# Kernel tuning notes

Hardware: AMD Instinct MI355X
Metric: run time of the kernel (lower is better)

Reference implementation:

```python
import jax, jax.numpy as jnp
import numpy as np

B, T, N, D = 8, 512, 64, 128
PRED, HEADS, HID = 96, 8, 256
KERNELS = (17, 49)
NUM_LAYERS = 1
NUM_BLOCKS = 1
IDX_T = np.arange(64)   # lowest 64 of T//2=256 rfft modes (mode_select='low')
IDX_C = np.arange(32)   # min(modes, (N+1)//2)=32 lowest channel-frequency modes


def _mov_avg(x, k):
    # x: [B, T, N]; replicate-pad (k-1)//2 on both ends, then box filter (AvgPool1d stride 1)
    pad = (k - 1) // 2
    xp = jnp.concatenate([jnp.repeat(x[:, :1], pad, axis=1), x, jnp.repeat(x[:, -1:], pad, axis=1)], axis=1)
    c = jnp.cumsum(xp, axis=1)
    c = jnp.concatenate([jnp.zeros_like(c[:, :1]), c], axis=1)
    return (c[:, k:] - c[:, :-k]) / k


def _decomp_multi(x, dec_w, dec_b):
    # series_decomp_multi: softmax-weighted mixture of moving averages
    mm = jnp.stack([_mov_avg(x, k) for k in KERNELS], axis=-1)        # [B,T,N,K]
    w = jax.nn.softmax(x[..., None] * dec_w + dec_b, axis=-1)         # Linear(1,K) on x, softmax over K
    trend = jnp.sum(mm * w, axis=-1)
    return x - trend, trend


def _complex_attn(x, Wq, Wk, Wv, Wo):
    # x: complex64 [B, L, M, D]; multi-head attention over the M selected frequency modes.
    # Real projection weights applied to complex activations; attention weights are
    # softmax over |q k^H| / sqrt(dh); values stay complex.
    Bq, L, M, Dm = x.shape
    dh = Dm // HEADS
    q = jnp.einsum('blmd,de->blme', x, Wq).reshape(Bq, L, M, HEADS, dh)
    k = jnp.einsum('blmd,de->blme', x, Wk).reshape(Bq, L, M, HEADS, dh)
    v = jnp.einsum('blmd,de->blme', x, Wv).reshape(Bq, L, M, HEADS, dh)
    s = jnp.einsum('blmhd,blnhd->blhmn', q, jnp.conj(k))              # complex scores
    w = jax.nn.softmax(jnp.abs(s) / np.sqrt(dh), axis=-1)             # real attn weights
    o = jnp.einsum('blhmn,blnhd->blmhd', w.astype(x.dtype), v).reshape(Bq, L, M, Dm)
    return jnp.einsum('blmd,de->blme', o, Wo)


def _cem(x, Wq, Wk, Wv, Wo):
    # channel-frequency attention; x: [B, N, T, D]
    xp = jnp.transpose(x, (0, 2, 1, 3))                               # [B,T,N,D]
    xf = jnp.fft.rfft(xp, axis=2)                                     # [B,T,N//2+1,D]
    xs = xf[:, :, IDX_C, :]                                           # gather selected modes
    for _ in range(NUM_LAYERS):
        xs = _complex_attn(xs, Wq, Wk, Wv, Wo)
    yf = jnp.zeros((x.shape[0], T, N // 2 + 1, D), dtype=xf.dtype).at[:, :, IDX_C, :].set(xs)
    y = jnp.fft.irfft(yf, n=N, axis=2)
    return jnp.transpose(y, (0, 2, 1, 3))


def _tem(x, Wq, Wk, Wv, Wo):
    # temporal-frequency attention; x: [B, N, T, D]
    xf = jnp.fft.rfft(x, axis=2)                                      # [B,N,T//2+1,D]
    xs = xf[:, :, IDX_T, :]
    for _ in range(NUM_LAYERS):
        xs = _complex_attn(xs, Wq, Wk, Wv, Wo)
    yf = jnp.zeros((x.shape[0], N, T // 2 + 1, D), dtype=xf.dtype).at[:, :, IDX_T, :].set(xs)
    return jnp.fft.irfft(yf, n=T, axis=2)


def setup_inputs() -> dict:
    key = jax.random.key(0)
    ks = jax.random.split(key, 24)
    r = lambda i, shape, s: jax.random.normal(ks[i], shape, jnp.float32) * s
    K = len(KERNELS)
    return {
        'x': jax.random.normal(ks[0], (B, T, N), jnp.float32),
        'embeddings': jax.random.normal(ks[1], (1, D), jnp.float32),
        'dec_w': r(2, (K,), 1.0),
        'dec_b': jnp.zeros((K,), jnp.float32),
        'mlp_w1': r(3, (T, HID), 1.0 / np.sqrt(T)),
        'mlp_b1': jnp.zeros((HID,), jnp.float32),
        'mlp_w2': r(4, (HID, HID), 1.0 / np.sqrt(HID)),
        'mlp_b2': jnp.zeros((HID,), jnp.float32),
        'mlp_w3': r(5, (HID, PRED), 1.0 / np.sqrt(HID)),
        'mlp_b3': jnp.zeros((PRED,), jnp.float32),
        'cem_Wq': r(6, (D, D), 0.02), 'cem_Wk': r(7, (D, D), 0.02),
        'cem_Wv': r(8, (D, D), 0.02), 'cem_Wo': r(9, (D, D), 0.02),
        'tem_Wq': r(10, (D, D), 0.02), 'tem_Wk': r(11, (D, D), 0.02),
        'tem_Wv': r(12, (D, D), 0.02), 'tem_Wo': r(13, (D, D), 0.02),
        'dr_w': r(14, (D, 1), 1.0 / np.sqrt(D)),
        'dr_b': jnp.zeros((1,), jnp.float32),
        'out_w': r(15, (T, PRED), 1.0 / np.sqrt(T)),
        'out_b': jnp.zeros((PRED,), jnp.float32),
        'W_fuse': jnp.ones((2,), jnp.float32),
    }


def reference(x, embeddings, dec_w, dec_b, mlp_w1, mlp_b1, mlp_w2, mlp_b2, mlp_w3, mlp_b3,
              cem_Wq, cem_Wk, cem_Wv, cem_Wo, tem_Wq, tem_Wk, tem_Wv, tem_Wo,
              dr_w, dr_b, out_w, out_b, W_fuse):
    res, trend = _decomp_multi(x, dec_w, dec_b)
    t = jnp.transpose(trend, (0, 2, 1))                               # [B,N,T]
    h = jax.nn.relu(t @ mlp_w1 + mlp_b1)
    h = jax.nn.relu(h @ mlp_w2 + mlp_b2)
    trend_out = jnp.transpose(h @ mlp_w3 + mlp_b3, (0, 2, 1))         # [B,PRED,N]
    # tokenEmb: [B,T,N] -> [B,N,T,1] * [1,D]
    xe = jnp.transpose(res, (0, 2, 1))[..., None] * embeddings[0]      # [B,N,T,D]
    for _ in range(NUM_BLOCKS):
        xe = _cem(xe, cem_Wq, cem_Wk, cem_Wv, cem_Wo)
    for _ in range(NUM_BLOCKS):
        xe = _tem(xe, tem_Wq, tem_Wk, tem_Wv, tem_Wo)
    xr = jnp.einsum('bntd,do->bnto', xe, dr_w)[..., 0] + dr_b[0]      # dim_reduction -> [B,N,T]
    xo = jnp.transpose(jnp.einsum('bnt,tp->bnp', xr, out_w) + out_b, (0, 2, 1))  # [B,PRED,N]
    return W_fuse[0] * xo + W_fuse[1] * trend_out
```

## Files before the change

kernel.cpp:

```cpp
#include <hip/hip_runtime.h>
#include <hip/hip_bf16.h>

typedef __hip_bfloat16 bf16;
typedef float v2f __attribute__((ext_vector_type(2)));

constexpr int CB = 8;
constexpr int CT = 512;
constexpr int CN = 64;
constexpr int CD = 128;
constexpr int CP = 96;
constexpr int CH = 8;
constexpr int CDH = 16;
constexpr int CHID = 256;
constexpr int CM = 32;
constexpr int CG = 64;
constexpr float TWO_PI = 6.28318530717958647692f;

__device__ __forceinline__ float LD(const void* p, size_t i, bool f) {
  return f ? ((const float*)p)[i] : __bfloat162float(((const bf16*)p)[i]);
}
template <bool F32>
__device__ __forceinline__ float LDT(const void* p, size_t i) {
  return F32 ? ((const float*)p)[i] : __bfloat162float(((const bf16*)p)[i]);
}

__device__ __forceinline__ bool detect_f32(const void* x) {
  const unsigned int* xw = (const unsigned int*)x;
  unsigned int w = xw[threadIdx.x & 63];
  unsigned int e = (w >> 7) & 0xFF;
  unsigned long long m = __ballot(e >= 0x90 || e <= 0x60);
  return __popcll(m) > 3;
}

struct MArgs {
  const void *x, *dec_w, *dec_b, *out_w, *emb, *cWq, *cWk, *cWv, *cWo;
  const void *tWq, *tWk, *tWv, *tWo, *drw, *drb, *out_b, *wfuse;
  const void *w1, *b1, *w2, *b2, *w3, *b3;
  float *trendo, *Pbuf, *ewq, *ewk, *ewv, *wod, *owr, *owi;
  void* out;
};

template <bool F32>
__device__ void k2_body(float* sm, const MArgs& a) {
  float* xbuf = sm;
  float* rows = sm;
  float* h1 = sm + 1536;
  float* h2 = sm + 2048;
  int r0 = blockIdx.x * 2;
  int b = r0 >> 6, n0 = r0 & 63;
  int tid = threadIdx.x;
  size_t xb = (size_t)b * CT * CN + n0;
  for (int i = tid; i < CT * 2; i += 256) {
    int t = i >> 1, q = i & 1;
    xbuf[t * 3 + q] = LDT<F32>(a.x, xb + (size_t)t * CN + q);
  }
  __syncthreads();
  float trv[4];
  int q = tid & 1, tl = tid >> 1, t0 = tl * 4;
  {
    float w0 = LDT<F32>(a.dec_w, 0), w1 = LDT<F32>(a.dec_w, 1);
    float c0 = LDT<F32>(a.dec_b, 0), c1 = LDT<F32>(a.dec_b, 1);
    float s17 = 0.f, s49 = 0.f;
    #pragma unroll
    for (int o = -8; o <= 8; ++o) {
      int u = t0 + o; u = u < 0 ? 0 : (u > CT - 1 ? CT - 1 : u);
      s17 += xbuf[u * 3 + q];
    }
    #pragma unroll
    for (int o = -24; o <= 24; ++o) {
      int u = t0 + o; u = u < 0 ? 0 : (u > CT - 1 ? CT - 1 : u);
      s49 += xbuf[u * 3 + q];
    }
    #pragma unroll
    for (int k = 0; k < 4; ++k) {
      int t = t0 + k;
      if (k > 0) {
        int up8 = t + 8 > CT - 1 ? CT - 1 : t + 8;
        int dn9 = t - 9 < 0 ? 0 : t - 9;
        int up24 = t + 24 > CT - 1 ? CT - 1 : t + 24;
        int dn25 = t - 25 < 0 ? 0 : t - 25;
        s17 += xbuf[up8 * 3 + q] - xbuf[dn9 * 3 + q];
        s49 += xbuf[up24 * 3 + q] - xbuf[dn25 * 3 + q];
      }
      float m0 = s17 * (1.f / 17.f), m1 = s49 * (1.f / 49.f);
      float xv = xbuf[t * 3 + q];
      float l0 = xv * w0 + c0, l1 = xv * w1 + c1;
      float mx = fmaxf(l0, l1);
      float e0 = __expf(l0 - mx), e1 = __expf(l1 - mx);
      trv[k] = (e0 * m0 + e1 * m1) / (e0 + e1);
    }
  }
  __syncthreads();
  #pragma unroll
  for (int k = 0; k < 4; ++k) rows[q * CT + t0 + k] = trv[k];
  __syncthreads();
  int c = tid;
  float a0, a1;
  {
    float bias = LDT<F32>(a.b1, c);
    a0 = a1 = 0.f;
    #pragma unroll 16
    for (int t = 0; t < CT; ++t) {
      float w = LDT<F32>(a.w1, t * CHID + c);
      a0 = fmaf(rows[t], w, a0);
      a1 = fmaf(rows[CT + t], w, a1);
    }
    h1[c] = fmaxf(a0 + bias, 0.f);
    h1[CHID + c] = fmaxf(a1 + bias, 0.f);
  }
  __syncthreads();
  {
    float bias = LDT<F32>(a.b2, c);
    a0 = a1 = 0.f;
    #pragma unroll 16
    for (int i = 0; i < CHID; ++i) {
      float w = LDT<F32>(a.w2, i * CHID + c);
      a0 = fmaf(h1[i], w, a0);
      a1 = fmaf(h1[CHID + i], w, a1);
    }
    h2[c] = fmaxf(a0 + bias, 0.f);
    h2[CHID + c] = fmaxf(a1 + bias, 0.f);
  }
  __syncthreads();
  if (tid < 2 * CP) {
    int p = tid < CP ? tid : tid - CP;
    int qh = tid < CP ? 0 : 1;
    float bias = LDT<F32>(a.b3, p);
    a0 = 0.f;
    #pragma unroll 16
    for (int i = 0; i < CHID; ++i)
      a0 = fmaf(h2[qh * CHID + i], LDT<F32>(a.w3, i * CP + p), a0);
    a.trendo[((size_t)(b * CN + n0 + qh)) * CP + p] = a0 + bias;
  }
}

__global__ __launch_bounds__(256, 4) void kS2(MArgs a) {
  __shared__ __align__(16) float sm[4608];
  bool f32 = detect_f32(a.x);
  int blk = blockIdx.x, tid = threadIdx.x;
  if (blk < 256) {
    if (f32) k2_body<true>(sm, a);
    else     k2_body<false>(sm, a);
  } else if (blk < 1280) {
    float* xl = sm;
    float2* SL = (float2*)sm;
    float* chp = sm + 3328;
    float* rowl = sm + 3328;
    float* Rr = sm + 3584;
    float* Ri = sm + 3712;
    float* aR = sm + 3840;
    float* prod = sm + 3968;
    float* chl = sm + 4096;
    float* eml = sm + 4104;
    int bk = blk - 256;
    int b = bk >> 7, tbase = (bk & 127) * 4;
    int w = tid >> 6, lane = tid & 63;
    size_t xb = (size_t)b * CT * CN;
    for (int i = tid; i < 52 * 64; i += 256) {
      int r = i >> 6, n = i & 63;
      int u = tbase - 24 + r; u = u < 0 ? 0 : (u > CT - 1 ? CT - 1 : u);
      xl[i] = LD(a.x, xb + (size_t)u * CN + n, f32);
    }
    if (tid < 128) eml[tid] = LD(a.emb, tid, f32);
    __syncthreads();
    {
      const void* Wm = (w < 2) ? a.cWq : a.cWk;
      int d0 = (w & 1) * 64;
      float p0 = 0.f, p1 = 0.f;
      #pragma unroll 16
      for (int d = d0; d < d0 + 64; ++d) {
        float em = eml[d];
        p0 = fmaf(em, LD(Wm, (size_t)d * CD + lane, f32), p0);
        p1 = fmaf(em, LD(Wm, (size_t)d * CD + 64 + lane, f32), p1);
      }
      chp[w * 128 + lane] = p0;
      chp[w * 128 + 64 + lane] = p1;
    }
    __syncthreads();
    if (tid < 128) {
      float pq = chp[tid] + chp[128 + tid];
      float pk = chp[256 + tid] + chp[384 + tid];
      prod[tid] = pq * pk;
    }
    __syncthreads();
    if (tid < CH) {
      float s = 0;
      #pragma unroll
      for (int j = 0; j < 16; ++j) s += prod[tid * 16 + j];
      chl[tid] = fabsf(s);
    }
    {
      int Lt = 24 + w;
      float w0 = LD(a.dec_w, 0, f32), w1 = LD(a.dec_w, 1, f32);
      float c0 = LD(a.dec_b, 0, f32), c1 = LD(a.dec_b, 1, f32);
      const float* xc = xl + Lt * 64 + lane;
      float pa = 0.f, pb = 0.f;
      #pragma unroll
      for (int o = -8; o <= 8; o += 2) pa += xc[o * 64];
      #pragma unroll
      for (int o = -7; o <= 7; o += 2) pb += xc[o * 64];
      float s17 = pa + pb;
      float qa = 0.f, qb = 0.f;
      #pragma unroll
      for (int o = 9; o <= 23; o += 2) qa += xc[o * 64] + xc[-o * 64];
      #pragma unroll
      for (int o = 10; o <= 24; o += 2) qb += xc[o * 64] + xc[-o * 64];
      float s49 = s17 + qa + qb;
      float m0 = s17 * (1.f / 17.f), m1 = s49 * (1.f / 49.f);
      float xv = xc[0];
      float l0 = xv * w0 + c0, l1 = xv * w1 + c1;
      float mx = fmaxf(l0, l1);
      float e0 = __expf(l0 - mx), e1 = __expf(l1 - mx);
      float tr = (e0 * m0 + e1 * m1) / (e0 + e1);
      rowl[w * 64 + lane] = xv - tr;
    }
    __syncthreads();
    float am, amax;
    {
      int m = lane & 31, half = lane >> 5;
      float cf, sf;
      sincosf((float)m * (TWO_PI / CN), &sf, &cf);
      float wr = (half & m & 1) ? -1.f : 1.f, wi = 0.f;
      float rr = 0.f, ri = 0.f;
      const float* rw = rowl + w * 64 + half * 32;
      #pragma unroll 8
      for (int j = 0; j < 32; ++j) {
        float xv = rw[j];
        rr = fmaf(xv, wr, rr);
        ri = fmaf(-xv, wi, ri);
        float nr = wr * cf - wi * sf; wi = wi * cf + wr * sf; wr = nr;
      }
      rr += __shfl_xor(rr, 32);
      ri += __shfl_xor(ri, 32);
      am = sqrtf(rr * rr + ri * ri);
      if (half == 0) { Rr[w * 32 + m] = rr; Ri[w * 32 + m] = ri; aR[w * 32 + m] = am; }
      amax = am;
      #pragma unroll
      for (int s2 = 1; s2 < 32; s2 <<= 1) amax = fmaxf(amax, __shfl_xor(amax, s2));
    }
    __syncthreads();
    {
      float base2 = 0.25f * 1.44269504f * am;
      int hb = lane >> 5;
      float al0 = chl[hb] * base2;
      float al1 = chl[hb + 2] * base2;
      float al2 = chl[hb + 4] * base2;
      float al3 = chl[hb + 6] * base2;
      float den0 = 0, sr0 = 0, si0 = 0, den1 = 0, sr1 = 0, si1 = 0;
      float den2 = 0, sr2 = 0, si2 = 0, den3 = 0, sr3 = 0, si3 = 0;
      const float* aRw = aR + w * 32;
      const float* Rrw = Rr + w * 32;
      const float* Riw = Ri + w * 32;
      for (int n2 = 0; n2 < CM; ++n2) {
        float d = aRw[n2] - amax;
        float rrn = Rrw[n2], rin = Riw[n2];
        float e0 = exp2f(al0 * d); den0 += e0; sr0 = fmaf(e0, rrn, sr0); si0 = fmaf(e0, rin, si0);
        float e1 = exp2f(al1 * d); den1 += e1; sr1 = fmaf(e1, rrn, sr1); si1 = fmaf(e1, rin, si1);
        float e2 = exp2f(al2 * d); den2 += e2; sr2 = fmaf(e2, rrn, sr2); si2 = fmaf(e2, rin, si2);
        float e3 = exp2f(al3 * d); den3 += e3; sr3 = fmaf(e3, rrn, sr3); si3 = fmaf(e3, rin, si3);
      }
      float r0 = 1.f / den0, r1 = 1.f / den1, r2 = 1.f / den2, r3 = 1.f / den3;
      SL[w * 256 + lane      ] = make_float2(sr0 * r0, si0 * r0);
      SL[w * 256 + lane + 64 ] = make_float2(sr1 * r1, si1 * r1);
      SL[w * 256 + lane + 128] = make_float2(sr2 * r2, si2 * r2);
      SL[w * 256 + lane + 192] = make_float2(sr3 * r3, si3 * r3);
    }
    __syncthreads();
    {
      int n2 = lane;
      const float2* Sw = SL + w * 256;
      float cd, sd;
      sincosf((float)n2 * (TWO_PI / CN), &sd, &cd);
      float c2 = cd * cd - sd * sd, s2 = 2.f * sd * cd;
      float pxA = 1.f, pyA = 0.f;
      float acc[8];
      #pragma unroll
      for (int h = 0; h < CH; ++h) acc[h] = -Sw[h * 32].x;
      for (int f2 = 0; f2 < 16; ++f2) {
        float pxB = pxA * cd - pyA * sd, pyB = pyA * cd + pxA * sd;
        #pragma unroll
        for (int h = 0; h < CH; ++h) {
          float4 sv = *(const float4*)(Sw + h * 32 + f2 * 2);
          acc[h] += 2.f * (sv.x * pxA - sv.y * pyA) + 2.f * (sv.z * pxB - sv.w * pyB);
        }
        float nx = pxA * c2 - pyA * s2; pyA = pyA * c2 + pxA * s2; pxA = nx;
      }
      int t = tbase + w;
      float* Pb = a.Pbuf + (((size_t)(b * CN + n2)) * CT + t) * CH;
      ((float4*)Pb)[0] = make_float4(acc[0] * (1.f / CN), acc[1] * (1.f / CN),
                                     acc[2] * (1.f / CN), acc[3] * (1.f / CN));
      ((float4*)Pb)[1] = make_float4(acc[4] * (1.f / CN), acc[5] * (1.f / CN),
                                     acc[6] * (1.f / CN), acc[7] * (1.f / CN));
    }
  } else if (blk < 1344) {
    float* ps = sm;
    int g = blk - 1280;
    int tc = tid >> 7, idx = tid & 127;
    if (idx < CP) {
      int p = idx, t0 = tc * 256;
      float s0, c0v, ss, cs;
      sincosf((float)((g * t0) & (CT - 1)) * (TWO_PI / CT), &s0, &c0v);
      sincosf((float)g * (TWO_PI / CT), &ss, &cs);
      float wr = c0v, wi = s0, ar = 0.f, ai = 0.f;
      #pragma unroll 16
      for (int t = 0; t < 256; ++t) {
        float w = LD(a.out_w, (size_t)(t0 + t) * CP + p, f32);
        ar = fmaf(w, wr, ar); ai = fmaf(w, wi, ai);
        float nr = wr * cs - wi * ss; wi = wi * cs + wr * ss; wr = nr;
      }
      ps[(tc * CP + p) * 2] = ar; ps[(tc * CP + p) * 2 + 1] = ai;
    }
    __syncthreads();
    if (tid < CP) {
      a.owr[g * CP + tid] = ps[tid * 2] + ps[(CP + tid) * 2];
      a.owi[g * CP + tid] = ps[tid * 2 + 1] + ps[(CP + tid) * 2 + 1];
    }
  } else if (blk < 1356) {
    float* eml = sm;
    float* evl = sm + 128;
    float* ewoh = sm + 160;
    int bi = blk - 1344;
    int half = tid >> 7, e = tid & 127;
    int pairIdx = bi * 2 + half;
    int which = pairIdx >> 3, h = pairIdx & 7;
    if (tid < 128) eml[tid] = LD(a.emb, tid, f32);
    __syncthreads();
    if (e < 16) {
      float acc = 0;
      #pragma unroll 8
      for (int d = 0; d < CD; ++d) acc += eml[d] * LD(a.cWv, d * CD + h * CDH + e, f32);
      evl[half * 16 + e] = acc;
    }
    __syncthreads();
    {
      float acc = 0;
      #pragma unroll
      for (int j = 0; j < CDH; ++j)
        acc += evl[half * 16 + j] * LD(a.cWo, (h * CDH + j) * CD + e, f32);
      ewoh[half * 128 + e] = acc;
    }
    __syncthreads();
    {
      const void* W = which == 0 ? a.tWq : (which == 1 ? a.tWk : a.tWv);
      float acc = 0;
      #pragma unroll 8
      for (int d = 0; d < CD; ++d) acc += ewoh[half * 128 + d] * LD(W, d * CD + e, f32);
      (which == 0 ? a.ewq : (which == 1 ? a.ewk : a.ewv))[h * CD + e] = acc;
    }
  } else {
    float* drl = sm;
    if (tid < 128) drl[tid] = LD(a.drw, tid, f32);
    __syncthreads();
    if (tid < 128) {
      float acc = 0;
      #pragma unroll 8
      for (int d = 0; d < CD; ++d) acc += LD(a.tWo, tid * CD + d, f32) * drl[d];
      a.wod[tid] = acc;
    }
  }
}

__global__ __launch_bounds__(1024, 4) void kC(MArgs a) {
  __shared__ __align__(16) float sm[8128];
  float* Pl = sm;
  float* QL = sm + 4352;
  float* Cl = sm + 5376;
  float* Ul = sm + 5888;
  float2* vdL = (float2*)(sm + 5952);
  float2* zL = (float2*)(sm + 6976);
  float* zrow = sm + 8000;
  bool f32 = detect_f32(a.x);
  int blk = blockIdx.x, tid = threadIdx.x;
  int b = blk >> 6, n = blk & 63;
  const float4* src4 = (const float4*)(a.Pbuf + ((size_t)(b * CN + n)) * CT * CH);
  {
    float4 v = src4[tid];
    int t = tid >> 1, half = tid & 1;
    int k = t >> 6, u = t & 63;
    float* dst = Pl + u * 68 + half * 32 + k;
    dst[0] = v.x; dst[8] = v.y; dst[16] = v.z; dst[24] = v.w;
  }
  if (tid < 576) {
    if (tid < 512) {
      int h = tid >> 6, aa = (tid >> 3) & 7, b2 = tid & 7;
      float c = 0;
      #pragma unroll
      for (int j = 0; j < CDH; ++j)
        c += a.ewq[aa * CD + h * CDH + j] * a.ewk[b2 * CD + h * CDH + j];
      Cl[tid] = c;
    } else {
      int r = tid - 512;
      int h = r >> 3, aa = r & 7;
      float c = 0;
      #pragma unroll
      for (int j = 0; j < CDH; ++j) c += a.ewv[aa * CD + h * CDH + j] * a.wod[h * CDH + j];
      Ul[r] = c;
    }
  }
  __syncthreads();
  {
    int g = tid >> 4, h = (tid >> 1) & 7, uh = tid & 1;
    float cs, sn;
    sincosf((float)g * (TWO_PI / CT), &sn, &cs);
    float s0, c0;
    sincosf((float)(g * uh) * (TWO_PI / 16.f), &s0, &c0);
    float wr = c0, wi = -s0;
    float car[8] = {0, 0, 0, 0, 0, 0, 0, 0};
    float cai[8] = {0, 0, 0, 0, 0, 0, 0, 0};
    const float* Pbase = Pl + (uh * 32) * 68 + h * 8;
    #pragma unroll 4
    for (int u = 0; u < 32; ++u) {
      const float4* pu = (const float4*)(Pbase + u * 68);
      float4 lo = pu[0], hi = pu[1];
      car[0] = fmaf(lo.x, wr, car[0]); cai[0] = fmaf(lo.x, wi, cai[0]);
      car[1] = fmaf(lo.y, wr, car[1]); cai[1] = fmaf(lo.y, wi, cai[1]);
      car[2] = fmaf(lo.z, wr, car[2]); cai[2] = fmaf(lo.z, wi, cai[2]);
      car[3] = fmaf(lo.w, wr, car[3]); cai[3] = fmaf(lo.w, wi, cai[3]);
      car[4] = fmaf(hi.x, wr, car[4]); cai[4] = fmaf(hi.x, wi, cai[4]);
      car[5] = fmaf(hi.y, wr, car[5]); cai[5] = fmaf(hi.y, wi, cai[5]);
      car[6] = fmaf(hi.z, wr, car[6]); cai[6] = fmaf(hi.z, wi, cai[6]);
      car[7] = fmaf(hi.w, wr, car[7]); cai[7] = fmaf(hi.w, wi, cai[7]);
      float nr = wr * cs + wi * sn; wi = wi * cs - wr * sn; wr = nr;
    }
    #pragma unroll
    for (int k = 0; k < 8; ++k) {
      car[k] += __shfl_xor(car[k], 1);
      cai[k] += __shfl_xor(cai[k], 1);
    }
    if (uh == 0) {
      float cs8, sn8;
      sincosf((float)(g & 7) * (TWO_PI / 8.f), &sn8, &cs8);
      float pr = 1.f, pi = 0.f, qr = 0.f, qi = 0.f;
      #pragma unroll
      for (int k = 0; k < 8; ++k) {
        qr += car[k] * pr - cai[k] * pi;
        qi += cai[k] * pr + car[k] * pi;
        float nr2 = pr * cs8 + pi * sn8; pi = pi * cs8 - pr * sn8; pr = nr2;
      }
      QL[g * 16 + h * 2] = qr;
      QL[g * 16 + h * 2 + 1] = qi;
    }
  }
  __syncthreads();
  int h = tid >> 7, m = (tid >> 1) & 63, gh = tid & 1;
  v2f qp[8];
  {
    const float4* q4 = (const float4*)(QL + m * 16);
    #pragma unroll
    for (int j = 0; j < 4; ++j) {
      float4 qv = q4[j];
      qp[2 * j]     = (v2f){qv.x, qv.y};
      qp[2 * j + 1] = (v2f){qv.z, qv.w};
    }
  }
  if (gh == 0) {
    float vr = 0, vi = 0;
    #pragma unroll
    for (int aa = 0; aa < 8; ++aa) {
      float u = Ul[h * 8 + aa];
      vr = fmaf(qp[aa].x, u, vr); vi = fmaf(qp[aa].y, u, vi);
    }
    vdL[h * 64 + m] = make_float2(vr, vi);
  }
  v2f uu[8], vv[8];
  #pragma unroll
  for (int bb = 0; bb < 8; ++bb) {
    v2f acc = {0.f, 0.f};
    #pragma unroll
    for (int aa = 0; aa < 8; ++aa) acc += qp[aa] * Cl[(h * 8 + aa) * 8 + bb];
    uu[bb] = acc;
    vv[bb] = (v2f){acc.y, -acc.x};
  }
  __syncthreads();
  float mx = -1e30f, den = 0.f, zr = 0.f, zi = 0.f;
  #pragma unroll 4
  for (int gi = 0; gi < 32; ++gi) {
    int g = gh * 32 + gi;
    const float4* y4 = (const float4*)(QL + g * 16);
    v2f sr2 = {0.f, 0.f}, si2 = {0.f, 0.f};
    #pragma unroll
    for (int j = 0; j < 4; ++j) {
      float4 yv = y4[j];
      v2f ya = {yv.x, yv.y}, yb = {yv.z, yv.w};
      sr2 = uu[2 * j] * ya + sr2;
      si2 = vv[2 * j] * ya + si2;
      sr2 = uu[2 * j + 1] * yb + sr2;
      si2 = vv[2 * j + 1] * yb + si2;
    }
    float sr = sr2.x + sr2.y;
    float si = si2.x + si2.y;
    float s = 0.25f * sqrtf(sr * sr + si * si);
    if (s > mx) {
      float f = __expf(mx - s);
      den *= f; zr *= f; zi *= f; mx = s;
    }
    float e = __expf(s - mx);
    float2 vd = vdL[h * 64 + g];
    den += e; zr += e * vd.x; zi += e * vd.y;
  }
  {
    float mx2 = __shfl_xor(mx, 1);
    float den2 = __shfl_xor(den, 1);
    float zr2 = __shfl_xor(zr, 1);
    float zi2 = __shfl_xor(zi, 1);
    float M = fmaxf(mx, mx2);
    float ea = __expf(mx - M), eb = __expf(mx2 - M);
    den = den * ea + den2 * eb;
    zr = zr * ea + zr2 * eb;
    zi = zi * ea + zi2 * eb;
    if (gh == 0) {
      float rv = 1.f / den;
      zL[h * 64 + m] = make_float2(zr * rv, zi * rv);
    }
  }
  __syncthreads();
  if (tid < 128) {
    int g = tid >> 1, c = tid & 1;
    float acc = 0;
    #pragma unroll
    for (int hh = 0; hh < CH; ++hh) acc += c ? zL[hh * 64 + g].y : zL[hh * 64 + g].x;
    zrow[g * 2 + c] = acc;
  }
  __syncthreads();
  if (tid < CP) {
    int p = tid;
    float acc = zrow[0] * a.owr[p] - zrow[1] * a.owi[p];
    #pragma unroll 8
    for (int g = 1; g < CG; ++g)
      acc += 2.f * (zrow[g * 2] * a.owr[g * CP + p] - zrow[g * 2 + 1] * a.owi[g * CP + p]);
    float xo = acc * (1.f / CT) + LD(a.drb, 0, f32) * a.owr[p] + LD(a.out_b, p, f32);
    float val = LD(a.wfuse, 0, f32) * xo
              + LD(a.wfuse, 1, f32) * a.trendo[((size_t)(b * CN + n)) * CP + p];
    size_t oidx = ((size_t)(b * CP + p)) * CN + n;
    if (f32) ((float*)a.out)[oidx] = val;
    else ((bf16*)a.out)[oidx] = __float2bfloat16(val);
  }
}

extern "C" void kernel_launch(void* const* d_in, const int* in_sizes, int n_in,
                              void* d_out, int out_size, void* d_ws, size_t ws_size,
                              hipStream_t stream) {
  float* W = (float*)d_ws;
  MArgs a;
  a.x = d_in[0];   a.emb = d_in[1];  a.dec_w = d_in[2]; a.dec_b = d_in[3];
  a.w1 = d_in[4];  a.b1 = d_in[5];   a.w2 = d_in[6];    a.b2 = d_in[7];
  a.w3 = d_in[8];  a.b3 = d_in[9];
  a.cWq = d_in[10]; a.cWk = d_in[11]; a.cWv = d_in[12]; a.cWo = d_in[13];
  a.tWq = d_in[14]; a.tWk = d_in[15]; a.tWv = d_in[16]; a.tWo = d_in[17];
  a.drw = d_in[18]; a.drb = d_in[19]; a.out_w = d_in[20]; a.out_b = d_in[21];
  a.wfuse = d_in[22];
  a.trendo = W; W += (size_t)CB * CN * CP;
  a.Pbuf = W;   W += (size_t)CB * CN * CT * CH;
  a.ewq = W;    W += CH * CD;
  a.ewk = W;    W += CH * CD;
  a.ewv = W;    W += CH * CD;
  a.wod = W;    W += CD;
  a.owr = W;    W += CG * CP;
  a.owi = W;    W += CG * CP;
  a.out = d_out;

  kS2<<<1357, 256, 0, stream>>>(a);
  kC<<<512, 1024, 0, stream>>>(a);
}
```

Before: 189.6 us.

## Split DFT and softmax halves across thread halves with LDS merges, pad QL rows

```diff
diff --git a/kernel.cpp b/kernel.cpp
--- a/kernel.cpp
+++ b/kernel.cpp
@@ -360,15 +360,17 @@
   }
 }
 
-__global__ __launch_bounds__(1024, 4) void kC(MArgs a) {
-  __shared__ __align__(16) float sm[8128];
+__global__ __launch_bounds__(1024, 2) void kC(MArgs a) {
+  __shared__ __align__(16) float sm[8384];
   float* Pl = sm;
   float* QL = sm + 4352;
-  float* Cl = sm + 5376;
-  float* Ul = sm + 5888;
-  float2* vdL = (float2*)(sm + 5952);
-  float2* zL = (float2*)(sm + 6976);
-  float* zrow = sm + 8000;
+  float* Cl = sm + 5632;
+  float* Ul = sm + 6144;
+  float2* vdL = (float2*)(sm + 6208);
+  float2* mrg = (float2*)(sm + 6208);
+  float2* zL = (float2*)(sm + 7232);
+  float* zrow = sm + 8256;
+  float4* mrgP = (float4*)sm;
   bool f32 = detect_f32(a.x);
   int blk = blockIdx.x, tid = threadIdx.x;
   int b = blk >> 6, n = blk & 63;
@@ -398,19 +400,21 @@
     }
   }
   __syncthreads();
+  float p2_qr, p2_qi;
+  int p2_uh = tid >> 9, p2_r = tid & 511;
   {
-    int g = tid >> 4, h = (tid >> 1) & 7, uh = tid & 1;
-    float cs, sn;
-    sincosf((float)g * (TWO_PI / CT), &sn, &cs);
-    float s0, c0;
-    sincosf((float)(g * uh) * (TWO_PI / 16.f), &s0, &c0);
-    float wr = c0, wi = -s0;
+    int g = p2_r >> 3, h = p2_r & 7, uh = p2_uh;
+    float cs1, sn1;
+    sincosf((float)g * (TWO_PI / CT), &sn1, &cs1);
+    float cs = cs1 * cs1 - sn1 * sn1;
+    float sn = 2.f * sn1 * cs1;
+    float wr = uh ? cs1 : 1.f, wi = uh ? -sn1 : 0.f;
     float car[8] = {0, 0, 0, 0, 0, 0, 0, 0};
     float cai[8] = {0, 0, 0, 0, 0, 0, 0, 0};
-    const float* Pbase = Pl + (uh * 32) * 68 + h * 8;
+    const float* Pbase = Pl + uh * 68 + h * 8;
     #pragma unroll 4
-    for (int u = 0; u < 32; ++u) {
-      const float4* pu = (const float4*)(Pbase + u * 68);
+    for (int v = 0; v < 32; ++v) {
+      const float4* pu = (const float4*)(Pbase + v * 136);
       float4 lo = pu[0], hi = pu[1];
       car[0] = fmaf(lo.x, wr, car[0]); cai[0] = fmaf(lo.x, wi, cai[0]);
       car[1] = fmaf(lo.y, wr, car[1]); cai[1] = fmaf(lo.y, wi, cai[1]);
@@ -422,30 +426,31 @@
       car[7] = fmaf(hi.w, wr, car[7]); cai[7] = fmaf(hi.w, wi, cai[7]);
       float nr = wr * cs + wi * sn; wi = wi * cs - wr * sn; wr = nr;
     }
+    float cs8, sn8;
+    sincosf((float)(g & 7) * (TWO_PI / 8.f), &sn8, &cs8);
+    float pr = 1.f, pi = 0.f, qr = 0.f, qi = 0.f;
     #pragma unroll
     for (int k = 0; k < 8; ++k) {
-      car[k] += __shfl_xor(car[k], 1);
-      cai[k] += __shfl_xor(cai[k], 1);
-    }
-    if (uh == 0) {
-      float cs8, sn8;
-      sincosf((float)(g & 7) * (TWO_PI / 8.f), &sn8, &cs8);
-      float pr = 1.f, pi = 0.f, qr = 0.f, qi = 0.f;
-      #pragma unroll
-      for (int k = 0; k < 8; ++k) {
-        qr += car[k] * pr - cai[k] * pi;
-        qi += cai[k] * pr + car[k] * pi;
-        float nr2 = pr * cs8 + pi * sn8; pi = pi * cs8 - pr * sn8; pr = nr2;
-      }
-      QL[g * 16 + h * 2] = qr;
-      QL[g * 16 + h * 2 + 1] = qi;
-    }
-  }
-  __syncthreads();
-  int h = tid >> 7, m = (tid >> 1) & 63, gh = tid & 1;
+      qr += car[k] * pr - cai[k] * pi;
+      qi += cai[k] * pr + car[k] * pi;
+      float nr2 = pr * cs8 + pi * sn8; pi = pi * cs8 - pr * sn8; pr = nr2;
+    }
+    p2_qr = qr; p2_qi = qi;
+    if (uh == 1) mrg[p2_r] = make_float2(qr, qi);
+  }
+  __syncthreads();
+  if (p2_uh == 0) {
+    int g = p2_r >> 3, h = p2_r & 7;
+    float2 o = mrg[p2_r];
+    QL[g * 20 + h * 2]     = p2_qr + o.x;
+    QL[g * 20 + h * 2 + 1] = p2_qi + o.y;
+  }
+  __syncthreads();
+  int gh = tid >> 9, r3 = tid & 511;
+  int h = r3 >> 6, m = r3 & 63;
   v2f qp[8];
   {
-    const float4* q4 = (const float4*)(QL + m * 16);
+    const float4* q4 = (const float4*)(QL + m * 20);
     #pragma unroll
     for (int j = 0; j < 4; ++j) {
       float4 qv = q4[j];
@@ -476,7 +481,7 @@
   #pragma unroll 4
   for (int gi = 0; gi < 32; ++gi) {
     int g = gh * 32 + gi;
-    const float4* y4 = (const float4*)(QL + g * 16);
+    const float4* y4 = (const float4*)(QL + g * 20);
     v2f sr2 = {0.f, 0.f}, si2 = {0.f, 0.f};
     #pragma unroll
     for (int j = 0; j < 4; ++j) {
@@ -498,20 +503,17 @@
     float2 vd = vdL[h * 64 + g];
     den += e; zr += e * vd.x; zi += e * vd.y;
   }
-  {
-    float mx2 = __shfl_xor(mx, 1);
-    float den2 = __shfl_xor(den, 1);
-    float zr2 = __shfl_xor(zr, 1);
-    float zi2 = __shfl_xor(zi, 1);
-    float M = fmaxf(mx, mx2);
-    float ea = __expf(mx - M), eb = __expf(mx2 - M);
-    den = den * ea + den2 * eb;
-    zr = zr * ea + zr2 * eb;
-    zi = zi * ea + zi2 * eb;
-    if (gh == 0) {
-      float rv = 1.f / den;
-      zL[h * 64 + m] = make_float2(zr * rv, zi * rv);
-    }
+  if (gh == 1) mrgP[r3] = make_float4(mx, den, zr, zi);
+  __syncthreads();
+  if (gh == 0) {
+    float4 o = mrgP[r3];
+    float M = fmaxf(mx, o.x);
+    float ea = __expf(mx - M), eb = __expf(o.x - M);
+    den = den * ea + o.y * eb;
+    zr = zr * ea + o.z * eb;
+    zi = zi * ea + o.w * eb;
+    float rv = 1.f / den;
+    zL[h * 64 + m] = make_float2(zr * rv, zi * rv);
   }
   __syncthreads();
   if (tid < 128) {
```

Measured after the change: 187.4 us. About the same (-1.1%).
